# Performance work log

Measured on AMD Instinct MI355X. Metric: run time of the kernel, lower is better.

## Reference

```python
import jax, jax.numpy as jnp
import numpy as np

B, S, DM = 4, 8192, 1024
N_RED = 16384   # tokens merged into their right neighbor
N_SAVE = 16384  # tokens kept; must be divisible by B


def setup_inputs() -> dict:
    key = jax.random.key(0)
    k1, k2, k3, k4 = jax.random.split(key, 4)
    x = jax.random.normal(k1, (B, S, DM), dtype=jnp.float32)
    W = jax.random.normal(k2, (DM, DM), dtype=jnp.float32) * (1.0 / np.sqrt(DM))
    ids_to_reduce = jax.random.randint(k3, (N_RED,), 0, B * S - 1, dtype=jnp.int64)
    ids_to_save = jax.random.randint(k4, (N_SAVE,), 0, B * S, dtype=jnp.int64)
    return {"x": x, "W": W, "ids_to_save": ids_to_save, "ids_to_reduce": ids_to_reduce}


def reference(x, W, ids_to_save, ids_to_reduce):
    batch_size, _, dm = x.shape
    xf = x.reshape(-1, dm)                       # [B*S, dm]
    reduced = xf[ids_to_reduce]                  # gather  [N_RED, dm]
    transformed = (reduced @ W.T).astype(jnp.float32)  # Linear, no bias
    xf = xf.at[ids_to_reduce + 1].add(transformed)     # scatter-add into right neighbor
    saved = xf[ids_to_save]                      # gather  [N_SAVE, dm]
    return saved.reshape(batch_size, -1, dm)     # [B, N_SAVE//B, dm]
```

## Files before the change

### kernel.cpp

```cpp
#include <hip/hip_runtime.h>

#define DM    1024
#define NTOK  32768
#define NRED  16384
#define NSAVE 16384
#define MMAX  16384

typedef __attribute__((ext_vector_type(8))) short bf16x8;
typedef __attribute__((ext_vector_type(4))) float f32x4;

__device__ __forceinline__ ushort f2bf(float f) {
    union { float f; unsigned u; } v; v.f = f;
    unsigned r = (v.u + 0x7FFF + ((v.u >> 16) & 1)) >> 16;
    return (ushort)r;
}
__device__ __forceinline__ float bf2f(ushort u) {
    union { unsigned u; float f; } v; v.u = ((unsigned)u) << 16;
    return v.f;
}

__global__ __launch_bounds__(256) void setup_kernel(const float* __restrict__ W,
                                                    ushort* __restrict__ Wb,
                                                    int* __restrict__ cnt,
                                                    int* __restrict__ need,
                                                    int* __restrict__ counter) {
    int t = blockIdx.x * 256 + threadIdx.x;
    float4 v = ((const float4*)W)[t];
    ushort4 o;
    o.x = f2bf(v.x); o.y = f2bf(v.y); o.z = f2bf(v.z); o.w = f2bf(v.w);
    ((ushort4*)Wb)[t] = o;
    if (t < NTOK) { cnt[t] = 0; need[t] = 0; }
    if (t == 0) *counter = 0;
}

__global__ __launch_bounds__(256) void prep_kernel(const int* __restrict__ red,
                                                   const int* __restrict__ sav,
                                                   int* __restrict__ cnt,
                                                   int* __restrict__ need) {
    int j = blockIdx.x * 256 + threadIdx.x;
    if (j >= NRED) return;
    atomicAdd(&cnt[red[j]], 1);
    int s = sav[j];
    if (s > 0) need[s - 1] = 1;
}

__global__ __launch_bounds__(256) void compact_kernel(const int* __restrict__ cnt,
                                                      const int* __restrict__ need,
                                                      int* __restrict__ inv,
                                                      int* __restrict__ list,
                                                      int* __restrict__ counter) {
    int t = blockIdx.x * 256 + threadIdx.x;
    if (t >= NTOK) return;
    if (need[t] && cnt[t] > 0) {
        int pos = atomicAdd(counter, 1);
        inv[t] = pos;
        list[pos] = t;
    }
}

__global__ __launch_bounds__(256) void convx_kernel(const float* __restrict__ X,
                                                    const int* __restrict__ list,
                                                    const int* __restrict__ counter,
                                                    ushort* __restrict__ Xb) {
    const int M = *counter;
    for (int r = blockIdx.x; r < M; r += gridDim.x) {
        int src = list[r];
        float4 v = ((const float4*)(X + (size_t)src * DM))[threadIdx.x];
        ushort4 o;
        o.x = f2bf(v.x); o.y = f2bf(v.y); o.z = f2bf(v.z); o.w = f2bf(v.w);
        ((ushort4*)(Xb + (size_t)r * DM))[threadIdx.x] = o;
    }
}

#define BM 128
#define BN 128
#define BK 32

__global__ __launch_bounds__(256) void gemm_kernel(const ushort* __restrict__ Xb,
                                                   const ushort* __restrict__ Wb,
                                                   const int* __restrict__ counter,
                                                   ushort* __restrict__ Tb) {
    const int M = *counter;
    const int m0 = blockIdx.x * BM;
    if (m0 >= M) return;
    const int n0 = blockIdx.y * BN;

    __shared__ ushort As[BM * BK];
    __shared__ ushort Bs[BN * BK];

    const int tid  = threadIdx.x;
    const int lane = tid & 63;
    const int wid  = tid >> 6;
    const int wr   = wid >> 1;
    const int wc   = wid & 1;
    const int kgrp = lane >> 4;
    const int r16  = lane & 15;

    const int srow  = tid >> 2;
    const int sslot = tid & 3;
    const int sw0 = (sslot ^ ((srow >> 1) & 3)) * 8;
    const int sw1 = (sslot ^ (((64 + srow) >> 1) & 3)) * 8;
    const ushort* aptr0 = Xb + (size_t)(m0 + srow) * DM + sw0;
    const ushort* aptr1 = Xb + (size_t)(m0 + 64 + srow) * DM + sw1;
    const ushort* bptr0 = Wb + (size_t)(n0 + srow) * DM + sw0;
    const ushort* bptr1 = Wb + (size_t)(n0 + 64 + srow) * DM + sw1;
    char* AsD = (char*)As + wid * 1024;
    char* BsD = (char*)Bs + wid * 1024;

    int aoff[4], boff[4];
#pragma unroll
    for (int fm = 0; fm < 4; ++fm) {
        int row = wr * 64 + fm * 16 + r16;
        aoff[fm] = row * BK + ((kgrp ^ ((row >> 1) & 3)) * 8);
    }
#pragma unroll
    for (int fn = 0; fn < 4; ++fn) {
        int row = wc * 64 + fn * 16 + r16;
        boff[fn] = row * BK + ((kgrp ^ ((row >> 1) & 3)) * 8);
    }

    f32x4 acc[4][4] = {};

    for (int k0 = 0; k0 < DM; k0 += BK) {
        __syncthreads();
        __builtin_amdgcn_global_load_lds(
            (const __attribute__((address_space(1))) unsigned*)(aptr0 + k0),
            (__attribute__((address_space(3))) unsigned*)(AsD), 16, 0, 0);
        __builtin_amdgcn_global_load_lds(
            (const __attribute__((address_space(1))) unsigned*)(aptr1 + k0),
            (__attribute__((address_space(3))) unsigned*)(AsD + 4096), 16, 0, 0);
        __builtin_amdgcn_global_load_lds(
            (const __attribute__((address_space(1))) unsigned*)(bptr0 + k0),
            (__attribute__((address_space(3))) unsigned*)(BsD), 16, 0, 0);
        __builtin_amdgcn_global_load_lds(
            (const __attribute__((address_space(1))) unsigned*)(bptr1 + k0),
            (__attribute__((address_space(3))) unsigned*)(BsD + 4096), 16, 0, 0);
        __syncthreads();

        bf16x8 af[4], bf[4];
#pragma unroll
        for (int i = 0; i < 4; ++i) af[i] = *(const bf16x8*)(As + aoff[i]);
#pragma unroll
        for (int j = 0; j < 4; ++j) bf[j] = *(const bf16x8*)(Bs + boff[j]);
#pragma unroll
        for (int i = 0; i < 4; ++i)
#pragma unroll
            for (int j = 0; j < 4; ++j)
                acc[i][j] = __builtin_amdgcn_mfma_f32_16x16x32_bf16(af[i], bf[j], acc[i][j], 0, 0, 0);
    }

#pragma unroll
    for (int fm = 0; fm < 4; ++fm) {
        int mbase = m0 + wr * 64 + fm * 16 + kgrp * 4;
#pragma unroll
        for (int fn = 0; fn < 4; ++fn) {
            int n = n0 + wc * 64 + fn * 16 + r16;
#pragma unroll
            for (int r = 0; r < 4; ++r) {
                int m = mbase + r;
                if (m < M) Tb[(size_t)m * DM + n] = f2bf(acc[fm][fn][r]);
            }
        }
    }
}

__global__ __launch_bounds__(256) void out_kernel(const float* __restrict__ X,
                                                  const ushort* __restrict__ Tb,
                                                  const int* __restrict__ sav,
                                                  const int* __restrict__ cnt,
                                                  const int* __restrict__ inv,
                                                  float* __restrict__ out) {
    int r = blockIdx.x;
    int d = threadIdx.x;
    int s = sav[r];
    const float4* xr = (const float4*)(X + (size_t)s * DM);
    float4 v = xr[d];
    if (s > 0) {
        int t = s - 1;
        int c = cnt[t];
        if (c > 0) {
            float fc = (float)c;
            const ushort4* tr = (const ushort4*)(Tb + (size_t)inv[t] * DM);
            ushort4 w = tr[d];
            v.x += fc * bf2f(w.x); v.y += fc * bf2f(w.y);
            v.z += fc * bf2f(w.z); v.w += fc * bf2f(w.w);
        }
    }
    ((float4*)out)[(size_t)r * (DM / 4) + d] = v;
}

extern "C" void kernel_launch(void* const* d_in, const int* in_sizes, int n_in,
                              void* d_out, int out_size, void* d_ws, size_t ws_size,
                              hipStream_t stream) {
    const float* X   = (const float*)d_in[0];
    const float* W   = (const float*)d_in[1];
    const int*   sav = (const int*)d_in[2];
    const int*   red = (const int*)d_in[3];
    float* out = (float*)d_out;

    char* ws = (char*)d_ws;
    int* counter = (int*)ws;
    int* cnt  = counter + 64;
    int* need = cnt + NTOK;
    int* inv  = need + NTOK;
    int* list = inv + NTOK;
    ushort* Wb = (ushort*)(ws + (1 << 19));
    ushort* Xb = (ushort*)(ws + (4 << 20));
    ushort* Tb = (ushort*)(ws + (36u << 20));

    setup_kernel<<<DM * DM / 4 / 256, 256, 0, stream>>>(W, Wb, cnt, need, counter);
    prep_kernel<<<NRED / 256, 256, 0, stream>>>(red, sav, cnt, need);
    compact_kernel<<<NTOK / 256, 256, 0, stream>>>(cnt, need, inv, list, counter);
    convx_kernel<<<2048, 256, 0, stream>>>(X, list, counter, Xb);

    dim3 ggrid(MMAX / BM, DM / BN);
    gemm_kernel<<<ggrid, 256, 0, stream>>>(Xb, Wb, counter, Tb);

    out_kernel<<<NSAVE, 256, 0, stream>>>(X, Tb, sav, cnt, inv, out);
}
```

Baseline: 76.83 us.

## Restructure GEMM as 64x64 split-K tiles with double-buffered LDS staging

The GEMM now uses 64x64 output tiles, with each of the four waves computing a split-K slice over a 128-wide K step. Partial sums are reduced through LDS in the epilogue. Global-to-LDS loads are double-buffered using explicit vmcnt waits so the next K chunk loads while MFMAs run, and rows past M are clamped. The aim is more blocks for the small, dynamic M and hidden load latency. In exchange it uses 64KB of LDS per block, which limits occupancy, and adds an LDS reduction step.

```diff
diff --git a/kernel.cpp b/kernel.cpp
--- a/kernel.cpp
+++ b/kernel.cpp
@@ -72,96 +72,112 @@
     }
 }
 
-#define BM 128
-#define BN 128
-#define BK 32
-
 __global__ __launch_bounds__(256) void gemm_kernel(const ushort* __restrict__ Xb,
                                                    const ushort* __restrict__ Wb,
                                                    const int* __restrict__ counter,
                                                    ushort* __restrict__ Tb) {
     const int M = *counter;
-    const int m0 = blockIdx.x * BM;
+    const int m0 = blockIdx.x * 64;
     if (m0 >= M) return;
-    const int n0 = blockIdx.y * BN;
-
-    __shared__ ushort As[BM * BK];
-    __shared__ ushort Bs[BN * BK];
+    const int n0 = blockIdx.y * 64;
+
+    __shared__ char lds[65536];
 
     const int tid  = threadIdx.x;
     const int lane = tid & 63;
-    const int wid  = tid >> 6;
-    const int wr   = wid >> 1;
-    const int wc   = wid & 1;
-    const int kgrp = lane >> 4;
-    const int r16  = lane & 15;
-
-    const int srow  = tid >> 2;
-    const int sslot = tid & 3;
-    const int sw0 = (sslot ^ ((srow >> 1) & 3)) * 8;
-    const int sw1 = (sslot ^ (((64 + srow) >> 1) & 3)) * 8;
-    const ushort* aptr0 = Xb + (size_t)(m0 + srow) * DM + sw0;
-    const ushort* aptr1 = Xb + (size_t)(m0 + 64 + srow) * DM + sw1;
-    const ushort* bptr0 = Wb + (size_t)(n0 + srow) * DM + sw0;
-    const ushort* bptr1 = Wb + (size_t)(n0 + 64 + srow) * DM + sw1;
-    char* AsD = (char*)As + wid * 1024;
-    char* BsD = (char*)Bs + wid * 1024;
+    const int w    = tid >> 6;
+
+    const ushort* a_src[4];
+    const ushort* b_src[4];
+#pragma unroll
+    for (int i = 0; i < 4; ++i) {
+        int q   = w * 256 + i * 64 + lane;
+        int row = q >> 4;
+        int c   = (q & 15) ^ (row & 7);
+        int ar  = m0 + row; if (ar >= M) ar = M - 1;
+        a_src[i] = Xb + (size_t)ar * DM + c * 8;
+        b_src[i] = Wb + (size_t)(n0 + row) * DM + c * 8;
+    }
+
+#define STAGE(buf, k0) do {                                                          \
+    char* _base = lds + (buf) * 32768 + w * 4096;                                    \
+    _Pragma("unroll")                                                                \
+    for (int _i = 0; _i < 4; ++_i) {                                                 \
+        __builtin_amdgcn_global_load_lds(                                            \
+            (const __attribute__((address_space(1))) unsigned*)(a_src[_i] + (k0)),   \
+            (__attribute__((address_space(3))) unsigned*)(_base + _i * 1024),        \
+            16, 0, 0);                                                               \
+        __builtin_amdgcn_global_load_lds(                                            \
+            (const __attribute__((address_space(1))) unsigned*)(b_src[_i] + (k0)),   \
+            (__attribute__((address_space(3))) unsigned*)(_base + 16384 + _i * 1024),\
+            16, 0, 0);                                                               \
+    }                                                                                \
+} while (0)
 
     int aoff[4], boff[4];
 #pragma unroll
-    for (int fm = 0; fm < 4; ++fm) {
-        int row = wr * 64 + fm * 16 + r16;
-        aoff[fm] = row * BK + ((kgrp ^ ((row >> 1) & 3)) * 8);
-    }
+    for (int f = 0; f < 4; ++f) {
+        int row = f * 16 + (lane & 15);
+        int c   = w * 4 + (lane >> 4);
+        int cp  = c ^ (row & 7);
+        aoff[f] = row * 256 + cp * 16;
+        boff[f] = row * 256 + cp * 16;
+    }
+
+    f32x4 acc[4][4] = {};
+
+    STAGE(0, 0);
+#pragma unroll
+    for (int t = 0; t < 8; ++t) {
+        const int cur = t & 1;
+        if (t < 7) {
+            STAGE(cur ^ 1, (t + 1) * 128);
+            asm volatile("s_waitcnt vmcnt(8)" ::: "memory");
+        } else {
+            asm volatile("s_waitcnt vmcnt(0)" ::: "memory");
+        }
+        __builtin_amdgcn_s_barrier();
+
+        const char* A = lds + cur * 32768;
+        const char* B = A + 16384;
+        bf16x8 af[4], bfr[4];
+#pragma unroll
+        for (int i = 0; i < 4; ++i) af[i]  = *(const bf16x8*)(A + aoff[i]);
+#pragma unroll
+        for (int j = 0; j < 4; ++j) bfr[j] = *(const bf16x8*)(B + boff[j]);
+#pragma unroll
+        for (int i = 0; i < 4; ++i)
+#pragma unroll
+            for (int j = 0; j < 4; ++j)
+                acc[i][j] = __builtin_amdgcn_mfma_f32_16x16x32_bf16(af[i], bfr[j], acc[i][j], 0, 0, 0);
+
+        asm volatile("s_waitcnt lgkmcnt(0)" ::: "memory");
+        __builtin_amdgcn_s_barrier();
+    }
+
+#pragma unroll
+    for (int fm = 0; fm < 4; ++fm)
+#pragma unroll
+        for (int fn = 0; fn < 4; ++fn) {
+            int F = fm * 4 + fn;
+            *(f32x4*)(lds + w * 16384 + lane * 256 + ((F ^ (lane & 15)) << 4)) = acc[fm][fn];
+        }
+    __syncthreads();
+
 #pragma unroll
     for (int fn = 0; fn < 4; ++fn) {
-        int row = wc * 64 + fn * 16 + r16;
-        boff[fn] = row * BK + ((kgrp ^ ((row >> 1) & 3)) * 8);
-    }
-
-    f32x4 acc[4][4] = {};
-
-    for (int k0 = 0; k0 < DM; k0 += BK) {
-        __syncthreads();
-        __builtin_amdgcn_global_load_lds(
-            (const __attribute__((address_space(1))) unsigned*)(aptr0 + k0),
-            (__attribute__((address_space(3))) unsigned*)(AsD), 16, 0, 0);
-        __builtin_amdgcn_global_load_lds(
-            (const __attribute__((address_space(1))) unsigned*)(aptr1 + k0),
-            (__attribute__((address_space(3))) unsigned*)(AsD + 4096), 16, 0, 0);
-        __builtin_amdgcn_global_load_lds(
-            (const __attribute__((address_space(1))) unsigned*)(bptr0 + k0),
-            (__attribute__((address_space(3))) unsigned*)(BsD), 16, 0, 0);
-        __builtin_amdgcn_global_load_lds(
-            (const __attribute__((address_space(1))) unsigned*)(bptr1 + k0),
-            (__attribute__((address_space(3))) unsigned*)(BsD + 4096), 16, 0, 0);
-        __syncthreads();
-
-        bf16x8 af[4], bf[4];
-#pragma unroll
-        for (int i = 0; i < 4; ++i) af[i] = *(const bf16x8*)(As + aoff[i]);
-#pragma unroll
-        for (int j = 0; j < 4; ++j) bf[j] = *(const bf16x8*)(Bs + boff[j]);
-#pragma unroll
-        for (int i = 0; i < 4; ++i)
-#pragma unroll
-            for (int j = 0; j < 4; ++j)
-                acc[i][j] = __builtin_amdgcn_mfma_f32_16x16x32_bf16(af[i], bf[j], acc[i][j], 0, 0, 0);
-    }
-
-#pragma unroll
-    for (int fm = 0; fm < 4; ++fm) {
-        int mbase = m0 + wr * 64 + fm * 16 + kgrp * 4;
-#pragma unroll
-        for (int fn = 0; fn < 4; ++fn) {
-            int n = n0 + wc * 64 + fn * 16 + r16;
-#pragma unroll
-            for (int r = 0; r < 4; ++r) {
-                int m = mbase + r;
-                if (m < M) Tb[(size_t)m * DM + n] = f2bf(acc[fm][fn][r]);
-            }
-        }
-    }
+        int F = w * 4 + fn;
+        f32x4 s = {0.f, 0.f, 0.f, 0.f};
+#pragma unroll
+        for (int sw = 0; sw < 4; ++sw)
+            s += *(const f32x4*)(lds + sw * 16384 + lane * 256 + ((F ^ (lane & 15)) << 4));
+        int n  = n0 + fn * 16 + (lane & 15);
+        int mb = m0 + w * 16 + (lane >> 4) * 4;
+#pragma unroll
+        for (int r = 0; r < 4; ++r)
+            if (mb + r < M) Tb[(size_t)(mb + r) * DM + n] = f2bf(s[r]);
+    }
+#undef STAGE
 }
 
 __global__ __launch_bounds__(256) void out_kernel(const float* __restrict__ X,
@@ -181,9 +197,9 @@
         if (c > 0) {
             float fc = (float)c;
             const ushort4* tr = (const ushort4*)(Tb + (size_t)inv[t] * DM);
-            ushort4 w = tr[d];
-            v.x += fc * bf2f(w.x); v.y += fc * bf2f(w.y);
-            v.z += fc * bf2f(w.z); v.w += fc * bf2f(w.w);
+            ushort4 wv = tr[d];
+            v.x += fc * bf2f(wv.x); v.y += fc * bf2f(wv.y);
+            v.z += fc * bf2f(wv.z); v.w += fc * bf2f(wv.w);
         }
     }
     ((float4*)out)[(size_t)r * (DM / 4) + d] = v;
@@ -213,7 +229,7 @@
     compact_kernel<<<NTOK / 256, 256, 0, stream>>>(cnt, need, inv, list, counter);
     convx_kernel<<<2048, 256, 0, stream>>>(X, list, counter, Xb);
 
-    dim3 ggrid(MMAX / BM, DM / BN);
+    dim3 ggrid(MMAX / 64, DM / 64);
     gemm_kernel<<<ggrid, 256, 0, stream>>>(Xb, Wb, counter, Tb);
 
     out_kernel<<<NSAVE, 256, 0, stream>>>(X, Tb, sav, cnt, inv, out);
```

Measured after the change: 73.69 us. 1.04x faster.
